# Optimization experiments

Measured on AMD Instinct MI355X. Metric: run time of the kernel, lower is better.

## Reference

```python
import jax, jax.numpy as jnp
import numpy as np

DY, DO, DI = 16, 256, 256
BS = 4096
EPS = 1e-6


def setup_inputs() -> dict:
    key = jax.random.key(0)
    k1, k2, k3, k4, k5 = jax.random.split(key, 5)
    k = 1.0 / float(np.sqrt(DY * DI))
    return {
        "x": jax.random.normal(k1, (DY * DI, BS), dtype=jnp.float32),
        "rms_params": jnp.ones((DY * DI,), dtype=jnp.float32)
        + 0.01 * jax.random.normal(k2, (DY * DI,), dtype=jnp.float32),
        "w_upper": jax.random.uniform(k3, (DY, DO, DI), minval=-k, maxval=k, dtype=jnp.float32),
        "w_lower": jax.random.uniform(k4, (DY, DO, DI), minval=-k, maxval=k, dtype=jnp.float32),
        "bias": jax.random.uniform(k5, (DY * DO,), minval=-k, maxval=k, dtype=jnp.float32),
    }


def reference(x, rms_params, w_upper, w_lower, bias):
    # x: (dy*di, bs) features-first layout, matching the torch op.
    dy, do, di = w_upper.shape
    bs = x.shape[1]
    # Per-column RMS factor (fc in the original op is shape (bs,)).
    fc = jax.lax.rsqrt(jnp.mean(x * x, axis=0) + EPS)  # (bs,)
    xn = x * rms_params[:, None] * fc[None, :]          # fused norm+scale
    xb = xn.reshape(dy, di, bs)
    # Dyadic structured matmul: upper acts on block d, lower on its paired
    # (reversed) block dy-1-d.
    up = jnp.einsum("doi,dib->dob", w_upper, xb)
    lo = jnp.einsum("doi,dib->dob", w_lower, xb[::-1])
    y = jax.nn.relu(up + lo + bias.reshape(dy, do, 1))
    return y.reshape(dy * do, bs)
```

## Files before the change

kernel.cpp:

```cpp
#include <hip/hip_runtime.h>

#define DYN 16
#define DON 256
#define DIN 256
#define BSN 4096
#define NF 4096
#define KTOT 512

typedef unsigned short u16;
typedef __attribute__((ext_vector_type(8))) short bf16x8;
typedef __attribute__((ext_vector_type(4))) float f32x4;
typedef __attribute__((ext_vector_type(4))) unsigned short u16x4;

static __device__ __forceinline__ u16 f2bf(float f) {
  unsigned u = __builtin_bit_cast(unsigned, f);
  u += 0x7fffu + ((u >> 16) & 1u);
  return (u16)(u >> 16);
}
static __device__ __forceinline__ float bf2f(u16 h) {
  unsigned u = ((unsigned)h) << 16;
  return __builtin_bit_cast(float, u);
}

__global__ __launch_bounds__(256) void k_pre(
    const float* __restrict__ x, const float* __restrict__ wu,
    const float* __restrict__ wl, const float* __restrict__ rms,
    u16* __restrict__ aprep, u16* __restrict__ xbf,
    float* __restrict__ partial) {
  __shared__ u16 tile[128 * 132];
  const int t = threadIdx.x;
  if (blockIdx.x < 1024) {
    int e = blockIdx.x * 256 + t;
    int row = e >> 6;
    int k0 = (e & 63) << 3;
    int d = row >> 8;
    const float* src;
    const float* rp;
    if (k0 < 256) {
      src = wu + (size_t)row * 256 + k0;
      rp  = rms + d * 256 + k0;
    } else {
      src = wl + (size_t)row * 256 + (k0 - 256);
      rp  = rms + (DYN - 1 - d) * 256 + (k0 - 256);
    }
    float4 s0 = *reinterpret_cast<const float4*>(src);
    float4 s1 = *reinterpret_cast<const float4*>(src + 4);
    float4 r0 = *reinterpret_cast<const float4*>(rp);
    float4 r1 = *reinterpret_cast<const float4*>(rp + 4);
    bf16x8 o;
    o[0] = (short)f2bf(s0.x * r0.x); o[1] = (short)f2bf(s0.y * r0.y);
    o[2] = (short)f2bf(s0.z * r0.z); o[3] = (short)f2bf(s0.w * r0.w);
    o[4] = (short)f2bf(s1.x * r1.x); o[5] = (short)f2bf(s1.y * r1.y);
    o[6] = (short)f2bf(s1.z * r1.z); o[7] = (short)f2bf(s1.w * r1.w);
    *reinterpret_cast<bf16x8*>(aprep + (size_t)row * KTOT + k0) = o;
    return;
  }
  const int bid = blockIdx.x - 1024;
  const int bt = bid & 31, ft = bid >> 5;
  const float* xb = x + (size_t)ft * 128 * BSN + bt * 128;
  const int frow = t >> 5, b4 = (t & 31) * 4;
  #pragma unroll
  for (int p = 0; p < 16; ++p) {
    int f = p * 8 + frow;
    float4 v = *reinterpret_cast<const float4*>(xb + (size_t)f * BSN + b4);
    u16x4 h;
    h[0] = f2bf(v.x); h[1] = f2bf(v.y); h[2] = f2bf(v.z); h[3] = f2bf(v.w);
    *reinterpret_cast<u16x4*>(&tile[f * 132 + b4]) = h;
  }
  __syncthreads();
  const int chunk = t & 15;
  const int bg = t >> 4;
  #pragma unroll
  for (int p = 0; p < 8; ++p) {
    int b = bg + p * 16;
    float s = 0.f;
    bf16x8 w;
    #pragma unroll
    for (int jj = 0; jj < 8; ++jj) {
      int j = (jj + chunk) & 7;
      u16 v = tile[(chunk * 8 + j) * 132 + b];
      float xv = bf2f(v);
      s += xv * xv;
      w[j] = (short)v;
    }
    *reinterpret_cast<bf16x8*>(
        xbf + (size_t)(bt * 128 + b) * NF + ft * 128 + chunk * 8) = w;
    #pragma unroll
    for (int m = 1; m < 16; m <<= 1) s += __shfl_xor(s, m, 64);
    if (chunk == 0) partial[ft * BSN + bt * 128 + b] = s;
  }
}

__global__ __launch_bounds__(512, 2) void k_gemm(
    const u16* __restrict__ aprep, const u16* __restrict__ xbf,
    const float* __restrict__ partial, const float* __restrict__ bias,
    float* __restrict__ out) {
  extern __shared__ char smem[];
  float* fcl = (float*)(smem + 98304);
  const int bid = blockIdx.x;
  const int dp = bid & 7;
  const int d = ((bid >> 3) & 1) ? (15 - dp) : dp;
  const int bt = bid >> 4;
  const int b0 = bt * 256;
  const int fr0 = d * 256;
  const int t = threadIdx.x;
  const int wave = t >> 6, lane = t & 63;
  const int lhi = lane >> 4, llo = lane & 15;
  const int wm = wave >> 2, wn = wave & 3;
  const int kmask = ((llo >> 1) & 7) << 4;

  f32x4 acc[8][4] = {};

  auto stage1 = [&](int slot, int kt, int op) {
    int j = op & 1;
    int c = j * 512 + t;
    int cl = c ^ ((c >> 3) & 7);
    int r = cl >> 2, kc = cl & 3;
    unsigned lbase = (unsigned)(slot * 32768 + (op >= 2 ? 16384 : 0) +
                                (j * 512 + wave * 64) * 16);
    const u16* g;
    if (op < 2) {
      int fbase = (kt < 8) ? (d * 256 + kt * 32)
                           : ((15 - d) * 256 + (kt - 8) * 32);
      g = xbf + (size_t)(b0 + r) * NF + fbase + kc * 8;
    } else {
      g = aprep + (size_t)(fr0 + r) * KTOT + kt * 32 + kc * 8;
    }
    __builtin_amdgcn_global_load_lds(
        (const __attribute__((address_space(1))) unsigned int*)g,
        (__attribute__((address_space(3))) unsigned int*)(smem + lbase),
        16, 0, 0);
  };
  auto stageK = [&](int slot, int kt) {
    #pragma unroll
    for (int op = 0; op < 4; ++op) stage1(slot, kt, op);
  };

  if (t < 256) {
    float fs = 0.f;
    #pragma unroll
    for (int i = 0; i < 32; ++i) fs += partial[i * BSN + b0 + t];
    fcl[t] = rsqrtf(fs * (1.0f / 4096.0f) + 1e-6f);
  }
  stageK(0, 0);
  stageK(1, 1);
  asm volatile("s_waitcnt vmcnt(4)\n\ts_barrier" ::: "memory");

  for (int kt = 0; kt < 16; ++kt) {
    const int slot = kt % 3;
    const char* sA = (const char*)smem + slot * 32768;
    const char* sB = sA + 16384;
    const int st_slot = (kt + 2) % 3;
    const bool do_st = kt < 14;
    bf16x8 af[4], bfr[4];

    #pragma unroll
    for (int j = 0; j < 4; ++j) {
      int row = wn * 64 + j * 16 + llo;
      bfr[j] = *reinterpret_cast<const bf16x8*>(sB + ((row * 64 + lhi * 16) ^ kmask));
    }
    #pragma unroll
    for (int i = 0; i < 4; ++i) {
      int row = wm * 128 + i * 16 + llo;
      af[i] = *reinterpret_cast<const bf16x8*>(sA + ((row * 64 + lhi * 16) ^ kmask));
    }
    if (do_st) { stage1(st_slot, kt + 2, 0); stage1(st_slot, kt + 2, 1); }
    asm volatile("" ::: "memory");
    __builtin_amdgcn_s_barrier();
    __builtin_amdgcn_s_setprio(1);
    #pragma unroll
    for (int i = 0; i < 4; ++i)
      #pragma unroll
      for (int j = 0; j < 4; ++j)
        acc[i][j] = __builtin_amdgcn_mfma_f32_16x16x32_bf16(af[i], bfr[j], acc[i][j], 0, 0, 0);
    __builtin_amdgcn_s_setprio(0);
    asm volatile("" ::: "memory");
    __builtin_amdgcn_s_barrier();

    #pragma unroll
    for (int i = 0; i < 4; ++i) {
      int row = wm * 128 + 64 + i * 16 + llo;
      af[i] = *reinterpret_cast<const bf16x8*>(sA + ((row * 64 + lhi * 16) ^ kmask));
    }
    if (do_st) { stage1(st_slot, kt + 2, 2); stage1(st_slot, kt + 2, 3); }
    asm volatile("" ::: "memory");
    __builtin_amdgcn_s_barrier();
    __builtin_amdgcn_s_setprio(1);
    #pragma unroll
    for (int i = 0; i < 4; ++i)
      #pragma unroll
      for (int j = 0; j < 4; ++j)
        acc[4 + i][j] = __builtin_amdgcn_mfma_f32_16x16x32_bf16(af[i], bfr[j], acc[4 + i][j], 0, 0, 0);
    __builtin_amdgcn_s_setprio(0);
    if (kt < 14) {
      asm volatile("s_waitcnt vmcnt(4)\n\ts_barrier" ::: "memory");
    } else if (kt == 14) {
      asm volatile("s_waitcnt vmcnt(0)\n\ts_barrier" ::: "memory");
    }
  }

  __syncthreads();
  float* esc = (float*)smem + wave * 2112;
  #pragma unroll
  for (int n = 0; n < 4; ++n) {
    int fo_l = wn * 64 + n * 16;
    float bv = bias[fr0 + fo_l + llo];
    #pragma unroll
    for (int m = 0; m < 8; ++m) {
      int lb = wm * 128 + m * 16 + lhi * 4;
      float4 fq = *reinterpret_cast<const float4*>(&fcl[lb]);
      float4 v;
      v.x = fmaxf(acc[m][n][0] * fq.x + bv, 0.f);
      v.y = fmaxf(acc[m][n][1] * fq.y + bv, 0.f);
      v.z = fmaxf(acc[m][n][2] * fq.z + bv, 0.f);
      v.w = fmaxf(acc[m][n][3] * fq.w + bv, 0.f);
      *reinterpret_cast<float4*>(&esc[llo * 132 + m * 16 + lhi * 4]) = v;
    }
    #pragma unroll
    for (int g = 0; g < 4; ++g) {
      int fl = g * 4 + lhi;
      size_t ob = (size_t)(fr0 + fo_l + fl) * BSN + b0 + wm * 128 + llo * 4;
      float4 v0 = *reinterpret_cast<const float4*>(&esc[fl * 132 + llo * 4]);
      float4 v1 = *reinterpret_cast<const float4*>(&esc[fl * 132 + 64 + llo * 4]);
      *reinterpret_cast<float4*>(out + ob) = v0;
      *reinterpret_cast<float4*>(out + ob + 64) = v1;
    }
  }
}

extern "C" void kernel_launch(void* const* d_in, const int* in_sizes, int n_in,
                              void* d_out, int out_size, void* d_ws, size_t ws_size,
                              hipStream_t stream) {
  (void)in_sizes; (void)n_in; (void)out_size; (void)ws_size;
  const float* x    = (const float*)d_in[0];
  const float* rms  = (const float*)d_in[1];
  const float* wu   = (const float*)d_in[2];
  const float* wl   = (const float*)d_in[3];
  const float* bias = (const float*)d_in[4];
  float* out = (float*)d_out;

  char* ws = (char*)d_ws;
  u16* xbf      = (u16*)ws;
  u16* aprep    = (u16*)(ws + 33554432);
  float* partial = (float*)(ws + 37748736);

  k_pre<<<2048, 256, 0, stream>>>(x, wu, wl, rms, aprep, xbf, partial);
  k_gemm<<<256, 512, 99328, stream>>>(aprep, xbf, partial, bias, out);
}
```

Measured before the change: 55.92 us.

## Split GEMM output tile into two halves, overlapping first-half stores with second-half compute

The 256x256 output tile per block is now computed as two sequential 256x128 halves, with a smaller 3-slot LDS ring (24 KB per slot) and half the accumulator registers. The first half's epilogue results are held in registers and written to global memory interleaved with the second half's K loop, so stores overlap MFMA work, and the LDS-staged transpose epilogue is replaced by direct float4 stores. The cost is that the B operand (xbf) is re-streamed from global memory twice per block, and the direct stores are less coalesced along the batch dimension.

```diff
diff --git a/kernel.cpp b/kernel.cpp
--- a/kernel.cpp
+++ b/kernel.cpp
@@ -96,44 +96,44 @@
     const float* __restrict__ partial, const float* __restrict__ bias,
     float* __restrict__ out) {
   extern __shared__ char smem[];
-  float* fcl = (float*)(smem + 98304);
+  float* fcl = (float*)(smem + 73728);
   const int bid = blockIdx.x;
   const int dp = bid & 7;
   const int d = ((bid >> 3) & 1) ? (15 - dp) : dp;
   const int bt = bid >> 4;
   const int b0 = bt * 256;
-  const int fr0 = d * 256;
   const int t = threadIdx.x;
   const int wave = t >> 6, lane = t & 63;
   const int lhi = lane >> 4, llo = lane & 15;
   const int wm = wave >> 2, wn = wave & 3;
   const int kmask = ((llo >> 1) & 7) << 4;
 
-  f32x4 acc[8][4] = {};
-
-  auto stage1 = [&](int slot, int kt, int op) {
-    int j = op & 1;
-    int c = j * 512 + t;
-    int cl = c ^ ((c >> 3) & 7);
-    int r = cl >> 2, kc = cl & 3;
-    unsigned lbase = (unsigned)(slot * 32768 + (op >= 2 ? 16384 : 0) +
-                                (j * 512 + wave * 64) * 16);
-    const u16* g;
-    if (op < 2) {
-      int fbase = (kt < 8) ? (d * 256 + kt * 32)
-                           : ((15 - d) * 256 + (kt - 8) * 32);
-      g = xbf + (size_t)(b0 + r) * NF + fbase + kc * 8;
-    } else {
-      g = aprep + (size_t)(fr0 + r) * KTOT + kt * 32 + kc * 8;
-    }
-    __builtin_amdgcn_global_load_lds(
-        (const __attribute__((address_space(1))) unsigned int*)g,
-        (__attribute__((address_space(3))) unsigned int*)(smem + lbase),
-        16, 0, 0);
-  };
-  auto stageK = [&](int slot, int kt) {
-    #pragma unroll
-    for (int op = 0; op < 4; ++op) stage1(slot, kt, op);
+  auto stage = [&](int slot, int kt, int frL) {
+    const int fbase = (kt < 8) ? (d * 256 + kt * 32)
+                               : ((15 - d) * 256 + (kt - 8) * 32);
+    #pragma unroll
+    for (int j = 0; j < 2; ++j) {
+      int c = j * 512 + t;
+      int cl = c ^ ((c >> 3) & 7);
+      int r = cl >> 2, kc = cl & 3;
+      const u16* g = xbf + (size_t)(b0 + r) * NF + fbase + kc * 8;
+      unsigned lbase = (unsigned)(slot * 24576 + (j * 512 + wave * 64) * 16);
+      __builtin_amdgcn_global_load_lds(
+          (const __attribute__((address_space(1))) unsigned int*)g,
+          (__attribute__((address_space(3))) unsigned int*)(smem + lbase),
+          16, 0, 0);
+    }
+    {
+      int c = t;
+      int cl = c ^ ((c >> 3) & 7);
+      int r = cl >> 2, kc = cl & 3;
+      const u16* g = aprep + (size_t)(frL + r) * KTOT + kt * 32 + kc * 8;
+      unsigned lbase = (unsigned)(slot * 24576 + 16384 + (wave * 64) * 16);
+      __builtin_amdgcn_global_load_lds(
+          (const __attribute__((address_space(1))) unsigned int*)g,
+          (__attribute__((address_space(3))) unsigned int*)(smem + lbase),
+          16, 0, 0);
+    }
   };
 
   if (t < 256) {
@@ -142,89 +142,95 @@
     for (int i = 0; i < 32; ++i) fs += partial[i * BSN + b0 + t];
     fcl[t] = rsqrtf(fs * (1.0f / 4096.0f) + 1e-6f);
   }
-  stageK(0, 0);
-  stageK(1, 1);
-  asm volatile("s_waitcnt vmcnt(4)\n\ts_barrier" ::: "memory");
-
-  for (int kt = 0; kt < 16; ++kt) {
-    const int slot = kt % 3;
-    const char* sA = (const char*)smem + slot * 32768;
-    const char* sB = sA + 16384;
-    const int st_slot = (kt + 2) % 3;
-    const bool do_st = kt < 14;
-    bf16x8 af[4], bfr[4];
-
-    #pragma unroll
-    for (int j = 0; j < 4; ++j) {
-      int row = wn * 64 + j * 16 + llo;
-      bfr[j] = *reinterpret_cast<const bf16x8*>(sB + ((row * 64 + lhi * 16) ^ kmask));
-    }
-    #pragma unroll
-    for (int i = 0; i < 4; ++i) {
-      int row = wm * 128 + i * 16 + llo;
-      af[i] = *reinterpret_cast<const bf16x8*>(sA + ((row * 64 + lhi * 16) ^ kmask));
-    }
-    if (do_st) { stage1(st_slot, kt + 2, 0); stage1(st_slot, kt + 2, 1); }
-    asm volatile("" ::: "memory");
-    __builtin_amdgcn_s_barrier();
-    __builtin_amdgcn_s_setprio(1);
-    #pragma unroll
-    for (int i = 0; i < 4; ++i)
-      #pragma unroll
-      for (int j = 0; j < 4; ++j)
-        acc[i][j] = __builtin_amdgcn_mfma_f32_16x16x32_bf16(af[i], bfr[j], acc[i][j], 0, 0, 0);
-    __builtin_amdgcn_s_setprio(0);
-    asm volatile("" ::: "memory");
-    __builtin_amdgcn_s_barrier();
-
-    #pragma unroll
-    for (int i = 0; i < 4; ++i) {
-      int row = wm * 128 + 64 + i * 16 + llo;
-      af[i] = *reinterpret_cast<const bf16x8*>(sA + ((row * 64 + lhi * 16) ^ kmask));
-    }
-    if (do_st) { stage1(st_slot, kt + 2, 2); stage1(st_slot, kt + 2, 3); }
-    asm volatile("" ::: "memory");
-    __builtin_amdgcn_s_barrier();
-    __builtin_amdgcn_s_setprio(1);
-    #pragma unroll
-    for (int i = 0; i < 4; ++i)
-      #pragma unroll
-      for (int j = 0; j < 4; ++j)
-        acc[4 + i][j] = __builtin_amdgcn_mfma_f32_16x16x32_bf16(af[i], bfr[j], acc[4 + i][j], 0, 0, 0);
-    __builtin_amdgcn_s_setprio(0);
-    if (kt < 14) {
-      asm volatile("s_waitcnt vmcnt(4)\n\ts_barrier" ::: "memory");
-    } else if (kt == 14) {
-      asm volatile("s_waitcnt vmcnt(0)\n\ts_barrier" ::: "memory");
-    }
-  }
-
-  __syncthreads();
-  float* esc = (float*)smem + wave * 2112;
+
+  f32x4 acc[8][2];
+  float4 e1[16];
+
   #pragma unroll
-  for (int n = 0; n < 4; ++n) {
-    int fo_l = wn * 64 + n * 16;
-    float bv = bias[fr0 + fo_l + llo];
+  for (int L = 0; L < 2; ++L) {
+    const int frL = d * 256 + L * 128;
+    #pragma unroll
+    for (int m = 0; m < 8; ++m)
+      #pragma unroll
+      for (int n = 0; n < 2; ++n)
+        acc[m][n] = f32x4{0.f, 0.f, 0.f, 0.f};
+
+    stage(0, 0, frL);
+    stage(1, 1, frL);
+    asm volatile("s_waitcnt vmcnt(3)\n\ts_barrier" ::: "memory");
+
+    #pragma unroll
+    for (int kt = 0; kt < 16; ++kt) {
+      const int slot = kt % 3;
+      const char* sA = (const char*)smem + slot * 24576;
+      const char* sB = sA + 16384;
+      if (L == 1) {
+        int m = kt >> 1, n = kt & 1;
+        size_t ob = (size_t)(d * 256 + wn * 32 + n * 16 + llo) * BSN +
+                    b0 + wm * 128 + m * 16 + lhi * 4;
+        *reinterpret_cast<float4*>(out + ob) = e1[kt];
+      }
+      if (kt < 14) stage((kt + 2) % 3, kt + 2, frL);
+
+      bf16x8 af[8], bq[2];
+      #pragma unroll
+      for (int m = 0; m < 8; ++m) {
+        int row = wm * 128 + m * 16 + llo;
+        af[m] = *reinterpret_cast<const bf16x8*>(
+            sA + ((row * 64 + lhi * 16) ^ kmask));
+      }
+      #pragma unroll
+      for (int n = 0; n < 2; ++n) {
+        int row = wn * 32 + n * 16 + llo;
+        bq[n] = *reinterpret_cast<const bf16x8*>(
+            sB + ((row * 64 + lhi * 16) ^ kmask));
+      }
+      __builtin_amdgcn_s_setprio(1);
+      #pragma unroll
+      for (int m = 0; m < 8; ++m)
+        #pragma unroll
+        for (int n = 0; n < 2; ++n)
+          acc[m][n] = __builtin_amdgcn_mfma_f32_16x16x32_bf16(
+              af[m], bq[n], acc[m][n], 0, 0, 0);
+      __builtin_amdgcn_s_setprio(0);
+
+      if (kt < 14) {
+        if (L == 1) {
+          asm volatile("s_waitcnt vmcnt(4)\n\ts_barrier" ::: "memory");
+        } else {
+          asm volatile("s_waitcnt vmcnt(3)\n\ts_barrier" ::: "memory");
+        }
+      } else if (kt == 14) {
+        if (L == 1) {
+          asm volatile("s_waitcnt vmcnt(1)\n\ts_barrier" ::: "memory");
+        } else {
+          asm volatile("s_waitcnt vmcnt(0)\n\ts_barrier" ::: "memory");
+        }
+      }
+    }
+
     #pragma unroll
     for (int m = 0; m < 8; ++m) {
       int lb = wm * 128 + m * 16 + lhi * 4;
       float4 fq = *reinterpret_cast<const float4*>(&fcl[lb]);
-      float4 v;
-      v.x = fmaxf(acc[m][n][0] * fq.x + bv, 0.f);
-      v.y = fmaxf(acc[m][n][1] * fq.y + bv, 0.f);
-      v.z = fmaxf(acc[m][n][2] * fq.z + bv, 0.f);
-      v.w = fmaxf(acc[m][n][3] * fq.w + bv, 0.f);
-      *reinterpret_cast<float4*>(&esc[llo * 132 + m * 16 + lhi * 4]) = v;
-    }
-    #pragma unroll
-    for (int g = 0; g < 4; ++g) {
-      int fl = g * 4 + lhi;
-      size_t ob = (size_t)(fr0 + fo_l + fl) * BSN + b0 + wm * 128 + llo * 4;
-      float4 v0 = *reinterpret_cast<const float4*>(&esc[fl * 132 + llo * 4]);
-      float4 v1 = *reinterpret_cast<const float4*>(&esc[fl * 132 + 64 + llo * 4]);
-      *reinterpret_cast<float4*>(out + ob) = v0;
-      *reinterpret_cast<float4*>(out + ob + 64) = v1;
-    }
+      #pragma unroll
+      for (int n = 0; n < 2; ++n) {
+        int fo = frL + wn * 32 + n * 16 + llo;
+        float bv = bias[fo];
+        float4 v;
+        v.x = fmaxf(acc[m][n][0] * fq.x + bv, 0.f);
+        v.y = fmaxf(acc[m][n][1] * fq.y + bv, 0.f);
+        v.z = fmaxf(acc[m][n][2] * fq.z + bv, 0.f);
+        v.w = fmaxf(acc[m][n][3] * fq.w + bv, 0.f);
+        if (L == 0) {
+          e1[m * 2 + n] = v;
+        } else {
+          *reinterpret_cast<float4*>(
+              out + (size_t)fo * BSN + b0 + lb) = v;
+        }
+      }
+    }
+    if (L == 0) __builtin_amdgcn_s_barrier();
   }
 }
 
@@ -245,5 +251,5 @@
   float* partial = (float*)(ws + 37748736);
 
   k_pre<<<2048, 256, 0, stream>>>(x, wu, wl, rms, aprep, xbf, partial);
-  k_gemm<<<256, 512, 99328, stream>>>(aprep, xbf, partial, bias, out);
-}
+  k_gemm<<<256, 512, 74752, stream>>>(aprep, xbf, partial, bias, out);
+}
```

After: 58.67 us. +4.9%, slower.
